# Performance work log

Hardware: AMD Instinct MI355X
Metric: run time of the kernel (lower is better)

The kernel has to match this reference:

```python
import jax, jax.numpy as jnp
import numpy as np

B, T, E, HID, V, K = 32, 512, 512, 512, 50257, 12
H = HID // 2          # per-direction LSTM hidden
START, STOP = 10, 11  # tag_to_ix['<START>'], tag_to_ix['<STOP>']
NEG = -10000.0


def setup_inputs() -> dict:
    key = jax.random.key(0)
    ks = jax.random.split(key, 16)
    sentence = jax.random.randint(ks[0], (B, T), 0, V)
    embed = jax.random.normal(ks[1], (V, E), jnp.float32) * 0.1
    # torch LSTM weights, gate order (i, f, g, o); biases fused (b_ih + b_hh)
    w_ih_f = jax.random.normal(ks[2], (4 * H, E), jnp.float32) * 0.05
    w_hh_f = jax.random.normal(ks[3], (4 * H, H), jnp.float32) * 0.05
    b_f = jax.random.normal(ks[4], (4 * H,), jnp.float32) * 0.05
    w_ih_b = jax.random.normal(ks[5], (4 * H, E), jnp.float32) * 0.05
    w_hh_b = jax.random.normal(ks[6], (4 * H, H), jnp.float32) * 0.05
    b_b = jax.random.normal(ks[7], (4 * H,), jnp.float32) * 0.05
    # init_hidden(): random initial states, [2 directions, B, H]
    h0 = jax.random.normal(ks[8], (2, B, H), jnp.float32)
    c0 = jax.random.normal(ks[9], (2, B, H), jnp.float32)
    W_out = jax.random.normal(ks[10], (K, HID), jnp.float32) * 0.05
    b_out = jax.random.normal(ks[11], (K,), jnp.float32) * 0.05
    transitions = jax.random.normal(ks[12], (K, K), jnp.float32)
    transitions = transitions.at[START, :].set(NEG).at[:, STOP].set(NEG)
    return dict(sentence=sentence, embed=embed,
                w_ih_f=w_ih_f, w_hh_f=w_hh_f, b_f=b_f,
                w_ih_b=w_ih_b, w_hh_b=w_hh_b, b_b=b_b,
                h0=h0, c0=c0, W_out=W_out, b_out=b_out,
                transitions=transitions)


def _lstm_dir(x, w_ih, w_hh, b, h0, c0, reverse):
    # x: [B, T, E] -> hidden sequence [B, T, H]
    xg = jnp.einsum('bte,ge->btg', x, w_ih) + b  # [B, T, 4H] input pre-activations

    def step(carry, xt):
        h, c = carry
        g = xt + h @ w_hh.T
        i, f, gg, o = jnp.split(g, 4, axis=-1)
        c = jax.nn.sigmoid(f) * c + jax.nn.sigmoid(i) * jnp.tanh(gg)
        h = jax.nn.sigmoid(o) * jnp.tanh(c)
        return (h, c), h

    _, ys = jax.lax.scan(step, (h0, c0), jnp.swapaxes(xg, 0, 1), reverse=reverse)
    return jnp.swapaxes(ys, 0, 1)


def reference(sentence, embed, w_ih_f, w_hh_f, b_f, w_ih_b, w_hh_b, b_b,
              h0, c0, W_out, b_out, transitions):
    # _get_lstm_features
    x = embed[sentence]  # [B, T, E]
    hf = _lstm_dir(x, w_ih_f, w_hh_f, b_f, h0[0], c0[0], False)
    hb = _lstm_dir(x, w_ih_b, w_hh_b, b_b, h0[1], c0[1], True)
    feats = jnp.concatenate([hf, hb], axis=-1) @ W_out.T + b_out  # [B, T, K]

    # _viterbi_decode: fused per-timestep max/argmax recurrence
    init = jnp.full((B, K), NEG, jnp.float32).at[:, START].set(0.0)

    def vstep(fv, feat_t):
        # scores[b, next, prev] = fv[b, prev] + transitions[next, prev]
        scores = fv[:, None, :] + transitions[None, :, :]
        bptr = jnp.argmax(scores, axis=2)            # [B, K]
        fv_new = jnp.max(scores, axis=2) + feat_t     # emit score added after max
        return fv_new, bptr

    fv, bptrs = jax.lax.scan(vstep, init, jnp.swapaxes(feats, 0, 1))  # bptrs [T, B, K]
    terminal = fv + transitions[STOP]                 # [B, K]
    best = jnp.argmax(terminal, axis=1)               # [B]
    # faithful to original: terminal_var[:, best_tag_id] -> [B, B]
    path_score = jnp.take(terminal, best, axis=1)

    def back(tag, bp):
        prev = jnp.take_along_axis(bp, tag[:, None], axis=1)[:, 0]
        return prev, prev

    _, ys = jax.lax.scan(back, best, bptrs, reverse=True)  # ys[t] = tag at position t-1
    # path positions 0..T-1 are (ys[1:], best); ys[0] is START (dropped by [:,1:])
    best_path = jnp.concatenate([ys[1:], best[None, :]], axis=0).T  # [B, T]
    return path_score, best_path
```

## Files before the change

### kernel.cpp

```cpp
#include <hip/hip_runtime.h>
#include <hip/hip_bf16.h>


typedef __attribute__((ext_vector_type(8))) __bf16 bf16x8;
typedef __attribute__((ext_vector_type(8))) unsigned short u16x8;
typedef __attribute__((ext_vector_type(4))) float  f32x4;

#define MFMA16(a, b, c) __builtin_amdgcn_mfma_f32_16x16x32_bf16((a), (b), (c), 0, 0, 0)

__device__ __forceinline__ float sigm(float x) { return 1.0f / (1.0f + __expf(-x)); }
__device__ __forceinline__ float tanh_f(float x) {
  x = fminf(fmaxf(x, -15.0f), 15.0f);
  float e = __expf(2.0f * x);
  return (e - 1.0f) / (e + 1.0f);
}

__device__ __forceinline__ void split8(const float* v, bf16x8& hi, bf16x8& lo) {
#pragma unroll
  for (int j = 0; j < 8; j++) {
    __bf16 h = (__bf16)v[j];
    hi[j] = h;
    lo[j] = (__bf16)(v[j] - (float)h);
  }
}

__global__ __launch_bounds__(256) void xg_gemm(
    const int* __restrict__ sent, const float* __restrict__ embed,
    const float* __restrict__ wih_f, const float* __restrict__ wih_b,
    const float* __restrict__ bias_f, const float* __restrict__ bias_b,
    float* __restrict__ xg)
{
  __shared__ __bf16 Ah[128][40], Al[128][40];
  __shared__ __bf16 Bh[128][40], Bl[128][40];
  __shared__ int toks[128];
  const int tid = threadIdx.x;
  const int m0 = blockIdx.x * 128, n0 = blockIdx.y * 128;
  if (tid < 128) toks[tid] = sent[m0 + tid];
  const int wave = tid >> 6, lane = tid & 63, q = lane >> 4, c = lane & 15;
  const int wy = wave >> 1, wx = wave & 1;
  f32x4 acc[4][4];
  for (int mt = 0; mt < 4; mt++)
    for (int nt = 0; nt < 4; nt++)
      acc[mt][nt] = f32x4{0.0f, 0.0f, 0.0f, 0.0f};
  __syncthreads();

  for (int k0 = 0; k0 < 512; k0 += 32) {
#pragma unroll
    for (int i = 0; i < 2; i++) {
      int ch = tid + (i << 8);
      int r = ch >> 2, kc = ch & 3;
      float tmp[8];
      const float* asrc = embed + (size_t)toks[r] * 512 + k0 + kc * 8;
#pragma unroll
      for (int j = 0; j < 8; j++) tmp[j] = asrc[j];
      bf16x8 hi, lo;
      split8(tmp, hi, lo);
      *(bf16x8*)&Ah[r][kc * 8] = hi;
      *(bf16x8*)&Al[r][kc * 8] = lo;
      int n = n0 + r;
      const float* wsrc = (n < 1024) ? (wih_f + (size_t)n * 512)
                                     : (wih_b + (size_t)(n - 1024) * 512);
#pragma unroll
      for (int j = 0; j < 8; j++) tmp[j] = wsrc[k0 + kc * 8 + j];
      split8(tmp, hi, lo);
      *(bf16x8*)&Bh[r][kc * 8] = hi;
      *(bf16x8*)&Bl[r][kc * 8] = lo;
    }
    __syncthreads();
    bf16x8 ah[4], al[4], bh[4], bl[4];
#pragma unroll
    for (int t4 = 0; t4 < 4; t4++) {
      int ar = wy * 64 + t4 * 16 + c, br = wx * 64 + t4 * 16 + c;
      ah[t4] = *(const bf16x8*)&Ah[ar][q * 8];
      al[t4] = *(const bf16x8*)&Al[ar][q * 8];
      bh[t4] = *(const bf16x8*)&Bh[br][q * 8];
      bl[t4] = *(const bf16x8*)&Bl[br][q * 8];
    }
#pragma unroll
    for (int mt = 0; mt < 4; mt++)
#pragma unroll
      for (int nt = 0; nt < 4; nt++) {
        acc[mt][nt] = MFMA16(ah[mt], bh[nt], acc[mt][nt]);
        acc[mt][nt] = MFMA16(al[mt], bh[nt], acc[mt][nt]);
        acc[mt][nt] = MFMA16(ah[mt], bl[nt], acc[mt][nt]);
      }
    __syncthreads();
  }

#pragma unroll
  for (int nt = 0; nt < 4; nt++) {
    int n = n0 + wx * 64 + nt * 16 + c;
    float bval = (n < 1024) ? bias_f[n] : bias_b[n - 1024];
#pragma unroll
    for (int mt = 0; mt < 4; mt++) {
      int mbase = m0 + wy * 64 + mt * 16 + q * 4;
#pragma unroll
      for (int reg = 0; reg < 4; reg++)
        xg[(size_t)(mbase + reg) * 2048 + n] = acc[mt][nt][reg] + bval;
    }
  }
}

__global__ __launch_bounds__(256, 1) void lstm_rec(
    const float* __restrict__ xg,
    const float* __restrict__ whh_f, const float* __restrict__ whh_b,
    const float* __restrict__ h0, const float* __restrict__ c0,
    float* __restrict__ h_seq,
    unsigned int* __restrict__ hx,
    int* __restrict__ flags)
{
  const int blk = blockIdx.x;
  const int d = blk >> 2, hs = blk & 3;
  const int tid = threadIdx.x;
  const int wave = tid >> 6, lane = tid & 63, q = lane >> 4, c = lane & 15;
  const float* __restrict__ whh = d ? whh_b : whh_f;

  __shared__ __bf16 hfrag[2][2][16][512];

  bf16x8 wfh[4][8], wfl[4][8];
#pragma unroll
  for (int g = 0; g < 4; g++) {
    int row = g * 256 + hs * 64 + wave * 16 + c;
    const float* wr = whh + (size_t)row * 256;
#pragma unroll
    for (int ks = 0; ks < 8; ks++) {
      float tmp[8];
#pragma unroll
      for (int j = 0; j < 8; j++) tmp[j] = wr[ks * 32 + q * 8 + j];
      split8(tmp, wfh[g][ks], wfl[g][ks]);
    }
  }
  const int ug = hs * 64 + wave * 16 + c;
  float cst[2][4];
#pragma unroll
  for (int mt = 0; mt < 2; mt++)
#pragma unroll
    for (int reg = 0; reg < 4; reg++)
      cst[mt][reg] = c0[d * 8192 + (mt * 16 + q * 4 + reg) * 256 + ug];

  const int sb = tid >> 3;
  const int kc4 = (tid & 7) * 4;

  auto load_xv = [&](float (&xv)[2][4][4], int tt) {
#pragma unroll
    for (int mt = 0; mt < 2; mt++)
#pragma unroll
      for (int reg = 0; reg < 4; reg++) {
        int b = mt * 16 + q * 4 + reg;
        const float* xr = xg + ((size_t)(b * 512 + tt) << 11) + (d << 10) + ug;
#pragma unroll
        for (int g = 0; g < 4; g++)
          xv[mt][g][reg] = xr[g << 8];
      }
  };

  float xv_cur[2][4][4];
  load_xv(xv_cur, d ? 511 : 0);

  for (int s = 0; s < 512; s++) {
    const int t_seq = d ? (511 - s) : s;
    const int p = s & 1;

    if (s == 0) {
#pragma unroll
      for (int i = 0; i < 4; i++) {
        int kc = kc4 + i;
        float tmp[8];
        const float* src = h0 + d * 8192 + sb * 256 + kc * 8;
#pragma unroll
        for (int j = 0; j < 8; j++) tmp[j] = src[j];
        bf16x8 vhi, vlo;
        split8(tmp, vhi, vlo);
        int fid = ((sb >> 4) << 3) + (kc >> 2);
        int cid = ((kc & 3) << 4) + (sb & 15);
        int pos = cid ^ (fid & 7);
        *(bf16x8*)&hfrag[0][0][fid][pos * 8] = vhi;
        *(bf16x8*)&hfrag[0][1][fid][pos * 8] = vlo;
      }
    } else {
      while (__hip_atomic_load(&flags[d * 512 + s - 1], __ATOMIC_RELAXED,
                               __HIP_MEMORY_SCOPE_AGENT) < 16)
        __builtin_amdgcn_s_sleep(1);

      const unsigned long long* hb64 = (const unsigned long long*)
          (hx + ((size_t)((d * 2 + p) * 32 + sb)) * 256 + kc4 * 8);
      unsigned long long v64[16];
#pragma unroll
      for (int i = 0; i < 16; i++)
        v64[i] = __hip_atomic_load(hb64 + i, __ATOMIC_RELAXED,
                                   __HIP_MEMORY_SCOPE_AGENT);
#pragma unroll
      for (int i = 0; i < 4; i++) {
        int kc = kc4 + i;
        u16x8 vhi, vlo;
#pragma unroll
        for (int j = 0; j < 8; j++) {
          unsigned long long dv = v64[i * 4 + (j >> 1)];
          unsigned int w32 = (j & 1) ? (unsigned int)(dv >> 32)
                                     : (unsigned int)dv;
          vhi[j] = (unsigned short)(w32 >> 16);
          vlo[j] = (unsigned short)(w32 & 0xffffu);
        }
        int fid = ((sb >> 4) << 3) + (kc >> 2);
        int cid = ((kc & 3) << 4) + (sb & 15);
        int pos = cid ^ (fid & 7);
        *(u16x8*)&hfrag[p][0][fid][pos * 8] = vhi;
        *(u16x8*)&hfrag[p][1][fid][pos * 8] = vlo;
      }
    }

    f32x4 acc[2][4];
#pragma unroll
    for (int mt = 0; mt < 2; mt++)
#pragma unroll
      for (int g = 0; g < 4; g++)
#pragma unroll
        for (int reg = 0; reg < 4; reg++)
          acc[mt][g][reg] = xv_cur[mt][g][reg];

    __syncthreads();

#pragma unroll
    for (int ks = 0; ks < 8; ks++) {
      int pos = (lane ^ ks) * 8;
      bf16x8 ahi0 = *(const bf16x8*)&hfrag[p][0][ks][pos];
      bf16x8 ahi1 = *(const bf16x8*)&hfrag[p][0][8 + ks][pos];
      bf16x8 alo0 = *(const bf16x8*)&hfrag[p][1][ks][pos];
      bf16x8 alo1 = *(const bf16x8*)&hfrag[p][1][8 + ks][pos];
#pragma unroll
      for (int g = 0; g < 4; g++) {
        acc[0][g] = MFMA16(ahi0, wfh[g][ks], acc[0][g]);
        acc[1][g] = MFMA16(ahi1, wfh[g][ks], acc[1][g]);
        acc[0][g] = MFMA16(alo0, wfh[g][ks], acc[0][g]);
        acc[1][g] = MFMA16(alo1, wfh[g][ks], acc[1][g]);
        acc[0][g] = MFMA16(ahi0, wfl[g][ks], acc[0][g]);
        acc[1][g] = MFMA16(ahi1, wfl[g][ks], acc[1][g]);
      }
    }

    const int pn = (s + 1) & 1;
    float hv[2][4];
#pragma unroll
    for (int mt = 0; mt < 2; mt++)
#pragma unroll
      for (int reg = 0; reg < 4; reg++) {
        int b = mt * 16 + q * 4 + reg;
        float iv = sigm(acc[mt][0][reg]);
        float fg = sigm(acc[mt][1][reg]);
        float gv = tanh_f(acc[mt][2][reg]);
        float ov = sigm(acc[mt][3][reg]);
        float cn = fg * cst[mt][reg] + iv * gv;
        cst[mt][reg] = cn;
        float hn = ov * tanh_f(cn);
        hv[mt][reg] = hn;
        __bf16 hhi = (__bf16)hn;
        __bf16 hlo = (__bf16)(hn - (float)hhi);
        unsigned int pack =
            ((unsigned int)__builtin_bit_cast(unsigned short, hhi) << 16) |
            (unsigned int)__builtin_bit_cast(unsigned short, hlo);
        __hip_atomic_store(&hx[((size_t)((d * 2 + pn) * 32 + b)) * 256 + ug], pack,
                           __ATOMIC_RELAXED, __HIP_MEMORY_SCOPE_AGENT);
      }

    asm volatile("s_waitcnt vmcnt(0)" ::: "memory");
    if (lane == 0)
      __hip_atomic_fetch_add(&flags[d * 512 + s], 1, __ATOMIC_RELAXED,
                             __HIP_MEMORY_SCOPE_AGENT);

#pragma unroll
    for (int mt = 0; mt < 2; mt++)
#pragma unroll
      for (int reg = 0; reg < 4; reg++) {
        int b = mt * 16 + q * 4 + reg;
        h_seq[((size_t)(b * 512 + t_seq) << 9) + (d << 8) + ug] = hv[mt][reg];
      }

    if (s < 511) {
      float xv_nxt[2][4][4];
      load_xv(xv_nxt, d ? (511 - (s + 1)) : (s + 1));
#pragma unroll
      for (int mt = 0; mt < 2; mt++)
#pragma unroll
        for (int g = 0; g < 4; g++)
#pragma unroll
          for (int reg = 0; reg < 4; reg++)
            xv_cur[mt][g][reg] = xv_nxt[mt][g][reg];
    }
  }
}

__global__ __launch_bounds__(256) void feats_k(
    const float* __restrict__ h_seq, const float* __restrict__ W_out,
    const float* __restrict__ b_out, float* __restrict__ feats)
{
  int m = blockIdx.x * 4 + (threadIdx.x >> 6);
  int lane = threadIdx.x & 63;
  const float4* hp = (const float4*)(h_seq + (size_t)m * 512 + lane * 8);
  float4 a = hp[0], b2 = hp[1];
  float h[8] = {a.x, a.y, a.z, a.w, b2.x, b2.y, b2.z, b2.w};
#pragma unroll
  for (int k = 0; k < 12; k++) {
    const float4* wp = (const float4*)(W_out + k * 512 + lane * 8);
    float4 w0 = wp[0], w1 = wp[1];
    float w[8] = {w0.x, w0.y, w0.z, w0.w, w1.x, w1.y, w1.z, w1.w};
    float p = 0.0f;
#pragma unroll
    for (int j = 0; j < 8; j++) p += h[j] * w[j];
#pragma unroll
    for (int off = 32; off > 0; off >>= 1) p += __shfl_xor(p, off);
    if (lane == 0) feats[(size_t)m * 12 + k] = p + b_out[k];
  }
}

__global__ __launch_bounds__(64) void viterbi_k(
    const float* __restrict__ feats, const float* __restrict__ trans,
    float* __restrict__ terminal, int* __restrict__ best,
    float* __restrict__ out_path)
{
  const int b = blockIdx.x;
  const int lane = threadIdx.x;
  __shared__ unsigned char bp[512][12];
  float trow[12];
#pragma unroll
  for (int pv = 0; pv < 12; pv++)
    trow[pv] = (lane < 12) ? trans[lane * 12 + pv] : -10000.0f;
  float fv = (lane == 10) ? 0.0f : -10000.0f;
  for (int t = 0; t < 512; t++) {
    float bestv = -3.4e38f;
    int arg = 0;
#pragma unroll
    for (int pv = 0; pv < 12; pv++) {
      float sc = __shfl(fv, pv) + trow[pv];
      if (sc > bestv) { bestv = sc; arg = pv; }
    }
    float ft = (lane < 12) ? feats[(size_t)(b * 512 + t) * 12 + lane] : 0.0f;
    if (lane < 12) {
      bp[t][lane] = (unsigned char)arg;
      fv = bestv + ft;
    }
  }
  float term = fv + ((lane < 12) ? trans[11 * 12 + lane] : 0.0f);
  if (lane < 12) terminal[b * 12 + lane] = term;
  float v = (lane < 12) ? term : -3.4e38f;
  int idx = lane;
#pragma unroll
  for (int off = 8; off > 0; off >>= 1) {
    float ov = __shfl_down(v, off);
    int oi = __shfl_down(idx, off);
    if (ov > v || (ov == v && oi < idx)) { v = ov; idx = oi; }
  }
  int bidx = __shfl(idx, 0);
  __syncthreads();
  if (lane == 0) {
    best[b] = bidx;
    int tag = bidx;
    out_path[b * 512 + 511] = (float)bidx;
    for (int t = 511; t >= 1; t--) {
      tag = bp[t][tag];
      out_path[b * 512 + t - 1] = (float)tag;
    }
  }
}

__global__ __launch_bounds__(256) void pscore_k(
    const float* __restrict__ terminal, const int* __restrict__ best,
    float* __restrict__ out)
{
  int idx = blockIdx.x * 256 + threadIdx.x;
  if (idx < 1024) {
    int i = idx >> 5, j = idx & 31;
    out[idx] = terminal[i * 12 + best[j]];
  }
}

extern "C" void kernel_launch(void* const* d_in, const int* in_sizes, int n_in,
                              void* d_out, int out_size, void* d_ws, size_t ws_size,
                              hipStream_t stream)
{
  const int*   sent  = (const int*)d_in[0];
  const float* embed = (const float*)d_in[1];
  const float* wih_f = (const float*)d_in[2];
  const float* whh_f = (const float*)d_in[3];
  const float* b_f   = (const float*)d_in[4];
  const float* wih_b = (const float*)d_in[5];
  const float* whh_b = (const float*)d_in[6];
  const float* b_b   = (const float*)d_in[7];
  const float* h0    = (const float*)d_in[8];
  const float* c0    = (const float*)d_in[9];
  const float* W_out = (const float*)d_in[10];
  const float* b_out = (const float*)d_in[11];
  const float* trans = (const float*)d_in[12];

  char* ws = (char*)d_ws;
  float*        xg    = (float*)(ws);
  float*        h_seq = (float*)(ws + 134217728);
  float*        feats = (float*)(ws + 167772160);
  unsigned int* hx    = (unsigned int*)(ws + 168558592);
  int*          flags = (int*)(ws + 168689664);
  float*        term  = (float*)(ws + 168693760);
  int*          best  = (int*)(ws + 168695296);

  float* outp = (float*)d_out;

  hipMemsetAsync(flags, 0, 2 * 512 * sizeof(int), stream);
  xg_gemm<<<dim3(128, 16), 256, 0, stream>>>(sent, embed, wih_f, wih_b, b_f, b_b, xg);
  lstm_rec<<<8, 256, 0, stream>>>(xg, whh_f, whh_b, h0, c0, h_seq, hx, flags);
  feats_k<<<4096, 256, 0, stream>>>(h_seq, W_out, b_out, feats);
  viterbi_k<<<32, 64, 0, stream>>>(feats, trans, term, best, outp + 1024);
  pscore_k<<<4, 256, 0, stream>>>(term, best, outp);
}
```

Before: 4.002 ms.

## Exchange LSTM hidden state via h_seq with per-block flags instead of packed buffer

Removes the separate packed bf16 hi/lo exchange buffer. Each block now writes fp32 h directly into h_seq with atomic stores, and readers split it into hi/lo themselves. The single global fetch_add counter per step becomes four per-block flag slots, set once all four waves finish through an LDS counter and polled with a wave-wide __all. This cuts duplicate global stores and atomic contention on the serial step path. In exchange, readers do more conversion work, and LDS double buffering is dropped, which relies on the __syncthreads ordering to stay correct.

```diff
diff --git a/kernel.cpp b/kernel.cpp
--- a/kernel.cpp
+++ b/kernel.cpp
@@ -3,7 +3,6 @@
 
 
 typedef __attribute__((ext_vector_type(8))) __bf16 bf16x8;
-typedef __attribute__((ext_vector_type(8))) unsigned short u16x8;
 typedef __attribute__((ext_vector_type(4))) float  f32x4;
 
 #define MFMA16(a, b, c) __builtin_amdgcn_mfma_f32_16x16x32_bf16((a), (b), (c), 0, 0, 0)
@@ -106,7 +105,6 @@
     const float* __restrict__ whh_f, const float* __restrict__ whh_b,
     const float* __restrict__ h0, const float* __restrict__ c0,
     float* __restrict__ h_seq,
-    unsigned int* __restrict__ hx,
     int* __restrict__ flags)
 {
   const int blk = blockIdx.x;
@@ -115,7 +113,10 @@
   const int wave = tid >> 6, lane = tid & 63, q = lane >> 4, c = lane & 15;
   const float* __restrict__ whh = d ? whh_b : whh_f;
 
-  __shared__ __bf16 hfrag[2][2][16][512];
+  __shared__ __bf16 hfrag[2][16][512];
+  __shared__ int lcnt;
+
+  if (tid == 0) lcnt = 0;
 
   bf16x8 wfh[4][8], wfl[4][8];
 #pragma unroll
@@ -159,7 +160,6 @@
 
   for (int s = 0; s < 512; s++) {
     const int t_seq = d ? (511 - s) : s;
-    const int p = s & 1;
 
     if (s == 0) {
 #pragma unroll
@@ -174,38 +174,43 @@
         int fid = ((sb >> 4) << 3) + (kc >> 2);
         int cid = ((kc & 3) << 4) + (sb & 15);
         int pos = cid ^ (fid & 7);
-        *(bf16x8*)&hfrag[0][0][fid][pos * 8] = vhi;
-        *(bf16x8*)&hfrag[0][1][fid][pos * 8] = vlo;
+        *(bf16x8*)&hfrag[0][fid][pos * 8] = vhi;
+        *(bf16x8*)&hfrag[1][fid][pos * 8] = vlo;
       }
     } else {
-      while (__hip_atomic_load(&flags[d * 512 + s - 1], __ATOMIC_RELAXED,
-                               __HIP_MEMORY_SCOPE_AGENT) < 16)
+      const int* fp = flags + ((d * 512 + (s - 1)) << 2) + (lane & 3);
+      int fv = __hip_atomic_load(fp, __ATOMIC_RELAXED, __HIP_MEMORY_SCOPE_AGENT);
+      while (!__all(fv == s)) {
         __builtin_amdgcn_s_sleep(1);
-
-      const unsigned long long* hb64 = (const unsigned long long*)
-          (hx + ((size_t)((d * 2 + p) * 32 + sb)) * 256 + kc4 * 8);
+        fv = __hip_atomic_load(fp, __ATOMIC_RELAXED, __HIP_MEMORY_SCOPE_AGENT);
+      }
+
+      const int t_prev = d ? (512 - s) : (s - 1);
+      const unsigned long long* hb = (const unsigned long long*)
+          (h_seq + ((size_t)(sb * 512 + t_prev) << 9) + (d << 8) + ((tid & 7) << 5));
       unsigned long long v64[16];
 #pragma unroll
       for (int i = 0; i < 16; i++)
-        v64[i] = __hip_atomic_load(hb64 + i, __ATOMIC_RELAXED,
+        v64[i] = __hip_atomic_load(hb + i, __ATOMIC_RELAXED,
                                    __HIP_MEMORY_SCOPE_AGENT);
 #pragma unroll
       for (int i = 0; i < 4; i++) {
         int kc = kc4 + i;
-        u16x8 vhi, vlo;
+        float f[8];
 #pragma unroll
         for (int j = 0; j < 8; j++) {
           unsigned long long dv = v64[i * 4 + (j >> 1)];
           unsigned int w32 = (j & 1) ? (unsigned int)(dv >> 32)
                                      : (unsigned int)dv;
-          vhi[j] = (unsigned short)(w32 >> 16);
-          vlo[j] = (unsigned short)(w32 & 0xffffu);
+          f[j] = __builtin_bit_cast(float, w32);
         }
+        bf16x8 vhi, vlo;
+        split8(f, vhi, vlo);
         int fid = ((sb >> 4) << 3) + (kc >> 2);
         int cid = ((kc & 3) << 4) + (sb & 15);
         int pos = cid ^ (fid & 7);
-        *(u16x8*)&hfrag[p][0][fid][pos * 8] = vhi;
-        *(u16x8*)&hfrag[p][1][fid][pos * 8] = vlo;
+        *(bf16x8*)&hfrag[0][fid][pos * 8] = vhi;
+        *(bf16x8*)&hfrag[1][fid][pos * 8] = vlo;
       }
     }
 
@@ -223,10 +228,10 @@
 #pragma unroll
     for (int ks = 0; ks < 8; ks++) {
       int pos = (lane ^ ks) * 8;
-      bf16x8 ahi0 = *(const bf16x8*)&hfrag[p][0][ks][pos];
-      bf16x8 ahi1 = *(const bf16x8*)&hfrag[p][0][8 + ks][pos];
-      bf16x8 alo0 = *(const bf16x8*)&hfrag[p][1][ks][pos];
-      bf16x8 alo1 = *(const bf16x8*)&hfrag[p][1][8 + ks][pos];
+      bf16x8 ahi0 = *(const bf16x8*)&hfrag[0][ks][pos];
+      bf16x8 ahi1 = *(const bf16x8*)&hfrag[0][8 + ks][pos];
+      bf16x8 alo0 = *(const bf16x8*)&hfrag[1][ks][pos];
+      bf16x8 alo1 = *(const bf16x8*)&hfrag[1][8 + ks][pos];
 #pragma unroll
       for (int g = 0; g < 4; g++) {
         acc[0][g] = MFMA16(ahi0, wfh[g][ks], acc[0][g]);
@@ -238,8 +243,6 @@
       }
     }
 
-    const int pn = (s + 1) & 1;
-    float hv[2][4];
 #pragma unroll
     for (int mt = 0; mt < 2; mt++)
 #pragma unroll
@@ -252,28 +255,19 @@
         float cn = fg * cst[mt][reg] + iv * gv;
         cst[mt][reg] = cn;
         float hn = ov * tanh_f(cn);
-        hv[mt][reg] = hn;
-        __bf16 hhi = (__bf16)hn;
-        __bf16 hlo = (__bf16)(hn - (float)hhi);
-        unsigned int pack =
-            ((unsigned int)__builtin_bit_cast(unsigned short, hhi) << 16) |
-            (unsigned int)__builtin_bit_cast(unsigned short, hlo);
-        __hip_atomic_store(&hx[((size_t)((d * 2 + pn) * 32 + b)) * 256 + ug], pack,
+        unsigned int hw = __builtin_bit_cast(unsigned int, hn);
+        __hip_atomic_store(
+            (unsigned int*)&h_seq[((size_t)(b * 512 + t_seq) << 9) + (d << 8) + ug],
+            hw, __ATOMIC_RELAXED, __HIP_MEMORY_SCOPE_AGENT);
+      }
+
+    asm volatile("s_waitcnt vmcnt(0)" ::: "memory");
+    if (lane == 0) {
+      int old = atomicAdd(&lcnt, 1);
+      if (old == 4 * s + 3)
+        __hip_atomic_store(&flags[((d * 512 + s) << 2) + hs], s + 1,
                            __ATOMIC_RELAXED, __HIP_MEMORY_SCOPE_AGENT);
-      }
-
-    asm volatile("s_waitcnt vmcnt(0)" ::: "memory");
-    if (lane == 0)
-      __hip_atomic_fetch_add(&flags[d * 512 + s], 1, __ATOMIC_RELAXED,
-                             __HIP_MEMORY_SCOPE_AGENT);
-
-#pragma unroll
-    for (int mt = 0; mt < 2; mt++)
-#pragma unroll
-      for (int reg = 0; reg < 4; reg++) {
-        int b = mt * 16 + q * 4 + reg;
-        h_seq[((size_t)(b * 512 + t_seq) << 9) + (d << 8) + ug] = hv[mt][reg];
-      }
+    }
 
     if (s < 511) {
       float xv_nxt[2][4][4];
@@ -392,19 +386,18 @@
   const float* trans = (const float*)d_in[12];
 
   char* ws = (char*)d_ws;
-  float*        xg    = (float*)(ws);
-  float*        h_seq = (float*)(ws + 134217728);
-  float*        feats = (float*)(ws + 167772160);
-  unsigned int* hx    = (unsigned int*)(ws + 168558592);
-  int*          flags = (int*)(ws + 168689664);
-  float*        term  = (float*)(ws + 168693760);
-  int*          best  = (int*)(ws + 168695296);
+  float* xg    = (float*)(ws);
+  float* h_seq = (float*)(ws + 134217728);
+  float* feats = (float*)(ws + 167772160);
+  int*   flags = (int*)(ws + 168558592);
+  float* term  = (float*)(ws + 168693760);
+  int*   best  = (int*)(ws + 168695296);
 
   float* outp = (float*)d_out;
 
-  hipMemsetAsync(flags, 0, 2 * 512 * sizeof(int), stream);
+  hipMemsetAsync(flags, 0, 2 * 512 * 4 * sizeof(int), stream);
   xg_gemm<<<dim3(128, 16), 256, 0, stream>>>(sent, embed, wih_f, wih_b, b_f, b_b, xg);
-  lstm_rec<<<8, 256, 0, stream>>>(xg, whh_f, whh_b, h0, c0, h_seq, hx, flags);
+  lstm_rec<<<8, 256, 0, stream>>>(xg, whh_f, whh_b, h0, c0, h_seq, flags);
   feats_k<<<4096, 256, 0, stream>>>(h_seq, W_out, b_out, feats);
   viterbi_k<<<32, 64, 0, stream>>>(feats, trans, term, best, outp + 1024);
   pscore_k<<<4, 256, 0, stream>>>(term, best, outp);
```

New measurement: 4.515 ms. 12.8% more time.
